# Kernel optimization log

Measured on AMD Instinct MI355X. Metric: run time of the kernel, lower is better.

The kernel has to match this reference:

```python
import jax, jax.numpy as jnp
import numpy as np

B, S, D = 32, 1024, 128
NUM_VT = 32
MIN_DR, MAX_DR = 0.0, 30.0
MIN_SOG, MAX_SOG = 0.0, 40.0
MIN_ROT, MAX_ROT = -127.0, 127.0


def setup_inputs() -> dict:
    key = jax.random.key(0)
    ks = jax.random.split(key, 32)
    u = lambda k, lo, hi: jax.random.uniform(k, (B, S, 1), minval=lo, maxval=hi, dtype=jnp.float32)
    lon = u(ks[0], -180.0, 180.0)
    lat = u(ks[1], -90.0, 90.0)
    rot = u(ks[2], MIN_ROT, MAX_ROT)
    sog = u(ks[3], MIN_SOG, MAX_SOG)
    cog = u(ks[4], 0.0, 360.0)
    head = u(ks[5], 0.0, 360.0)
    vtype = jax.random.randint(ks[6], (B, S, 1), 0, NUM_VT).astype(jnp.float32)
    dr = u(ks[7], MIN_DR, MAX_DR)
    ais_data = jnp.concatenate([lon, lat, rot, sog, cog, head, vtype, dr], axis=-1)
    p = lambda k, shape: (jax.random.normal(k, shape, dtype=jnp.float32) * 0.05)
    return {
        "ais_data": ais_data,
        "W_lon1": p(ks[8], (2, D)), "b_lon1": p(ks[9], (D,)),
        "W_lon2": p(ks[10], (D, D)), "b_lon2": p(ks[11], (D,)),
        "W_lat1": p(ks[12], (2, D)), "b_lat1": p(ks[13], (D,)),
        "W_lat2": p(ks[14], (D, D)), "b_lat2": p(ks[15], (D,)),
        "W_cog": p(ks[16], (2, D)), "b_cog": p(ks[17], (D,)),
        "W_head": p(ks[18], (2, D)), "b_head": p(ks[19], (D,)),
        "W_dr": p(ks[20], (1, D)), "b_dr": p(ks[21], (D,)),
        "W_sog": p(ks[22], (1, D)), "b_sog": p(ks[23], (D,)),
        "W_rot": p(ks[24], (1, D)), "b_rot": p(ks[25], (D,)),
        "emb": p(ks[26], (NUM_VT, D)),
    }


def reference(ais_data, W_lon1, b_lon1, W_lon2, b_lon2, W_lat1, b_lat1, W_lat2, b_lat2,
              W_cog, b_cog, W_head, b_head, W_dr, b_dr, W_sog, b_sog, W_rot, b_rot, emb):
    deg2rad = jnp.pi / 180.0
    lon = ais_data[..., 0:1]
    lat = ais_data[..., 1:2]
    rot = ais_data[..., 2:3]
    sog = ais_data[..., 3:4]
    cog = ais_data[..., 4:5]
    head = ais_data[..., 5:6]
    vtype = ais_data[..., 6]
    dr = ais_data[..., 7:8]

    def coord(x, mask_val, W1, b1, W2, b2):
        # x: [b,s,1] degrees -> 2-layer MLP on [sin, cos]
        xr = x * deg2rad
        f = jnp.concatenate([jnp.sin(xr), jnp.cos(xr)], axis=-1)  # [b,s,2]
        e = jax.nn.relu(f @ W1 + b1) @ W2 + b2                    # [b,s,D]
        return jnp.where(x == mask_val, 0.0, e)

    def cyclical(x, W, b):
        xr = x * deg2rad - jnp.pi
        f = jnp.concatenate([jnp.sin(xr), jnp.cos(xr)], axis=-1)
        e = f @ W + b
        return jnp.where(x == -1.0, 0.0, e)

    def continuous(x, mn, mx, W, b):
        xn = 2.0 * (x - mn) / jnp.maximum(mx - mn, 1e-6) - 1.0
        e = jnp.tanh(xn @ W + b)
        return jnp.where(x == -1.0, 0.0, e)

    enc_lon = coord(lon, 181.0, W_lon1, b_lon1, W_lon2, b_lon2)
    enc_lat = coord(lat, 91.0, W_lat1, b_lat1, W_lat2, b_lat2)
    enc_rot = continuous(rot, MIN_ROT, MAX_ROT, W_rot, b_rot)
    enc_sog = continuous(sog, MIN_SOG, MAX_SOG, W_sog, b_sog)
    enc_cog = cyclical(cog, W_cog, b_cog)
    enc_head = cyclical(head, W_head, b_head)
    vt_idx = jax.lax.stop_gradient(vtype).astype(jnp.int32)
    enc_vt = emb[vt_idx]                                          # [b,s,D]
    enc_dr = continuous(dr, MIN_DR, MAX_DR, W_dr, b_dr)

    # order matches torch.cat((spatial(lon,lat), rot, sog, cog, heading, vessel_type, draught))
    out = jnp.stack([enc_lon, enc_lat, enc_rot, enc_sog, enc_cog, enc_head, enc_vt, enc_dr], axis=2)
    b, s = ais_data.shape[:2]
    return out.reshape(b, s, -1)  # [b, s, 8*D]
```

## Files before the change

kernel.cpp:

```cpp
#include <hip/hip_runtime.h>
#include <cstdint>

typedef short bf16x8 __attribute__((ext_vector_type(8)));
typedef float f32x4 __attribute__((ext_vector_type(4)));

#define D2R 0.017453292519943295f
#define PI_F 3.14159265838979323846f
#undef PI_F
#define PI_F 3.14159265358979323846f

__device__ __forceinline__ unsigned bf16r(float x) {
    unsigned u = __float_as_uint(x);
    return (u + 0x7fffu + ((u >> 16) & 1u)) >> 16;
}

__device__ __forceinline__ float tanh_fast(float x) {
    float e = __expf(2.0f * x);
    return 1.0f - 2.0f / (e + 1.0f);
}

__global__ __launch_bounds__(512, 4) void hae_kernel(
    const float* __restrict__ ais,
    const float* __restrict__ Wlon1, const float* __restrict__ blon1,
    const float* __restrict__ Wlon2, const float* __restrict__ blon2,
    const float* __restrict__ Wlat1, const float* __restrict__ blat1,
    const float* __restrict__ Wlat2, const float* __restrict__ blat2,
    const float* __restrict__ Wcog,  const float* __restrict__ bcog,
    const float* __restrict__ Whead, const float* __restrict__ bhead,
    const float* __restrict__ Wdr,   const float* __restrict__ bdr,
    const float* __restrict__ Wsog,  const float* __restrict__ bsog,
    const float* __restrict__ Wrot,  const float* __restrict__ brot,
    const float* __restrict__ emb,
    float* __restrict__ out)
{
    __shared__ unsigned short hlds[2][64][128];
    __shared__ float s_sin[2][64], s_cos[2][64], s_mask[2][64];
    __shared__ float s_xn[3][64], s_mxn[3][64];
    __shared__ float s_scyc[2][64], s_ccyc[2][64], s_mcyc[2][64];
    __shared__ int   s_vt[64];

    const int t = threadIdx.x;
    const int tok0 = blockIdx.x * 64;

    if (t < 64) {
        const float* a = ais + (size_t)(tok0 + t) * 8;
        f32x4 a0 = *(const f32x4*)a;
        f32x4 a1 = *(const f32x4*)(a + 4);
        float lon = a0[0], lat = a0[1], rot = a0[2], sog = a0[3];
        float cog = a1[0], head = a1[1], vt = a1[2], dr = a1[3];

        float lr = lon * D2R;
        s_sin[0][t] = __sinf(lr); s_cos[0][t] = __cosf(lr);
        s_mask[0][t] = (lon == 181.0f) ? 0.f : 1.f;
        float tr = lat * D2R;
        s_sin[1][t] = __sinf(tr); s_cos[1][t] = __cosf(tr);
        s_mask[1][t] = (lat == 91.0f) ? 0.f : 1.f;

        s_xn[0][t] = (rot + 127.0f) * (2.0f / 254.0f) - 1.0f;
        s_mxn[0][t] = (rot == -1.0f) ? 0.f : 1.f;
        s_xn[1][t] = sog * (2.0f / 40.0f) - 1.0f;
        s_mxn[1][t] = (sog == -1.0f) ? 0.f : 1.f;
        s_xn[2][t] = dr * (2.0f / 30.0f) - 1.0f;
        s_mxn[2][t] = (dr == -1.0f) ? 0.f : 1.f;

        float cr = cog * D2R - PI_F;
        s_scyc[0][t] = __sinf(cr); s_ccyc[0][t] = __cosf(cr);
        s_mcyc[0][t] = (cog == -1.0f) ? 0.f : 1.f;
        float hr = head * D2R - PI_F;
        s_scyc[1][t] = __sinf(hr); s_ccyc[1][t] = __cosf(hr);
        s_mcyc[1][t] = (head == -1.0f) ? 0.f : 1.f;
        s_vt[t] = (int)vt;
    }
    __syncthreads();

    {
        const int j0 = (t & 63) * 2;
        const int quad = t >> 6;
        float w00a = Wlon1[j0],       w00b = Wlon1[j0 + 1];
        float w01a = Wlon1[128 + j0], w01b = Wlon1[128 + j0 + 1];
        float b0a  = blon1[j0],       b0b  = blon1[j0 + 1];
        float w10a = Wlat1[j0],       w10b = Wlat1[j0 + 1];
        float w11a = Wlat1[128 + j0], w11b = Wlat1[128 + j0 + 1];
        float b1a  = blat1[j0],       b1b  = blat1[j0 + 1];
        char* base0 = (char*)&hlds[0][0][0];
        char* base1 = (char*)&hlds[1][0][0];
        #pragma unroll
        for (int p = 0; p < 8; ++p) {
            int i = quad + p * 8;
            int sw = (j0 * 2) ^ ((i & 7) << 4);
            float s0 = s_sin[0][i], c0 = s_cos[0][i];
            float h0 = fmaxf(fmaf(s0, w00a, fmaf(c0, w01a, b0a)), 0.f);
            float h1 = fmaxf(fmaf(s0, w00b, fmaf(c0, w01b, b0b)), 0.f);
            *(unsigned*)(base0 + i * 256 + sw) = bf16r(h0) | (bf16r(h1) << 16);
            float s1 = s_sin[1][i], c1 = s_cos[1][i];
            float g0 = fmaxf(fmaf(s1, w10a, fmaf(c1, w11a, b1a)), 0.f);
            float g1 = fmaxf(fmaf(s1, w10b, fmaf(c1, w11b, b1b)), 0.f);
            *(unsigned*)(base1 + i * 256 + sw) = bf16r(g0) | (bf16r(g1) << 16);
        }
    }

    {
        const int d4 = (t & 31) * 4;
        const int io = t >> 5;
        f32x4 wr  = *(const f32x4*)(Wrot + d4),        br_ = *(const f32x4*)(brot + d4);
        f32x4 wsg = *(const f32x4*)(Wsog + d4),        bs_ = *(const f32x4*)(bsog + d4);
        f32x4 wdd = *(const f32x4*)(Wdr + d4),         bd_ = *(const f32x4*)(bdr + d4);
        f32x4 wc0 = *(const f32x4*)(Wcog + d4),  wc1 = *(const f32x4*)(Wcog + 128 + d4),  bc_ = *(const f32x4*)(bcog + d4);
        f32x4 wh0 = *(const f32x4*)(Whead + d4), wh1 = *(const f32x4*)(Whead + 128 + d4), bh_ = *(const f32x4*)(bhead + d4);
        #pragma unroll
        for (int p = 0; p < 4; ++p) {
            int i = io + p * 16;
            float* ob = out + (size_t)(tok0 + i) * 1024;
            {
                float xn = s_xn[0][i], mk = s_mxn[0][i];
                f32x4 v;
                #pragma unroll
                for (int e = 0; e < 4; ++e) v[e] = tanh_fast(fmaf(xn, wr[e], br_[e])) * mk;
                *(f32x4*)(ob + 2 * 128 + d4) = v;
            }
            {
                float xn = s_xn[1][i], mk = s_mxn[1][i];
                f32x4 v;
                #pragma unroll
                for (int e = 0; e < 4; ++e) v[e] = tanh_fast(fmaf(xn, wsg[e], bs_[e])) * mk;
                *(f32x4*)(ob + 3 * 128 + d4) = v;
            }
            {
                float sc = s_scyc[0][i], cc = s_ccyc[0][i], mk = s_mcyc[0][i];
                f32x4 v;
                #pragma unroll
                for (int e = 0; e < 4; ++e) v[e] = fmaf(sc, wc0[e], fmaf(cc, wc1[e], bc_[e])) * mk;
                *(f32x4*)(ob + 4 * 128 + d4) = v;
            }
            {
                float sc = s_scyc[1][i], cc = s_ccyc[1][i], mk = s_mcyc[1][i];
                f32x4 v;
                #pragma unroll
                for (int e = 0; e < 4; ++e) v[e] = fmaf(sc, wh0[e], fmaf(cc, wh1[e], bh_[e])) * mk;
                *(f32x4*)(ob + 5 * 128 + d4) = v;
            }
            {
                f32x4 ev = *(const f32x4*)(emb + (size_t)s_vt[i] * 128 + d4);
                *(f32x4*)(ob + 6 * 128 + d4) = ev;
            }
            {
                float xn = s_xn[2][i], mk = s_mxn[2][i];
                f32x4 v;
                #pragma unroll
                for (int e = 0; e < 4; ++e) v[e] = tanh_fast(fmaf(xn, wdd[e], bd_[e])) * mk;
                *(f32x4*)(ob + 7 * 128 + d4) = v;
            }
        }
    }

    const int w  = t >> 6;
    const int l  = t & 63;
    const int c  = w & 1;
    const int nh = (w >> 1) & 1;
    const int dq = w >> 2;
    const float* W2  = c ? Wlat2 : Wlon2;
    const float* b2p = c ? blat2 : blon2;
    const int col = l & 15;
    const int q   = l >> 4;
    const int dbase0 = nh * 64 + dq * 32;

    bf16x8 afrag[2][4];
    f32x4  bb4[2];
    #pragma unroll
    for (int dt = 0; dt < 2; ++dt) {
        const int dbase = dbase0 + dt * 16;
        bb4[dt] = *(const f32x4*)(b2p + dbase + q * 4);
        #pragma unroll
        for (int ks = 0; ks < 4; ++ks) {
            bf16x8 af;
            #pragma unroll
            for (int e = 0; e < 8; ++e)
                af[e] = (short)bf16r(W2[(size_t)(ks * 32 + q * 8 + e) * 128 + dbase + col]);
            afrag[dt][ks] = af;
        }
    }
    __syncthreads();

    char* hb = (char*)&hlds[c][0][0];
    #pragma unroll
    for (int tt = 0; tt < 4; ++tt) {
        const int brow = tt * 16 + col;
        const int swr = (brow & 7) << 4;
        bf16x8 bfrag[4];
        #pragma unroll
        for (int ks = 0; ks < 4; ++ks) {
            int jb = (ks * 32 + q * 8) * 2;
            bfrag[ks] = *(bf16x8*)(hb + brow * 256 + (jb ^ swr));
        }
        const float msk = s_mask[c][brow];
        float* op = out + (size_t)(tok0 + brow) * 1024 + c * 128 + dbase0 + q * 4;
        #pragma unroll
        for (int dt = 0; dt < 2; ++dt) {
            f32x4 acc = (f32x4){0.f, 0.f, 0.f, 0.f};
            acc = __builtin_amdgcn_mfma_f32_16x16x32_bf16(afrag[dt][0], bfrag[0], acc, 0, 0, 0);
            acc = __builtin_amdgcn_mfma_f32_16x16x32_bf16(afrag[dt][1], bfrag[1], acc, 0, 0, 0);
            acc = __builtin_amdgcn_mfma_f32_16x16x32_bf16(afrag[dt][2], bfrag[2], acc, 0, 0, 0);
            acc = __builtin_amdgcn_mfma_f32_16x16x32_bf16(afrag[dt][3], bfrag[3], acc, 0, 0, 0);
            f32x4 v;
            #pragma unroll
            for (int r = 0; r < 4; ++r) v[r] = (acc[r] + bb4[dt][r]) * msk;
            *(f32x4*)(op + dt * 16) = v;
        }
    }
}

extern "C" void kernel_launch(void* const* d_in, const int* in_sizes, int n_in,
                              void* d_out, int out_size, void* d_ws, size_t ws_size,
                              hipStream_t stream) {
    (void)in_sizes; (void)n_in; (void)d_ws; (void)ws_size; (void)out_size;
    const float* ais   = (const float*)d_in[0];
    const float* Wlon1 = (const float*)d_in[1];
    const float* blon1 = (const float*)d_in[2];
    const float* Wlon2 = (const float*)d_in[3];
    const float* blon2 = (const float*)d_in[4];
    const float* Wlat1 = (const float*)d_in[5];
    const float* blat1 = (const float*)d_in[6];
    const float* Wlat2 = (const float*)d_in[7];
    const float* blat2 = (const float*)d_in[8];
    const float* Wcog  = (const float*)d_in[9];
    const float* bcog  = (const float*)d_in[10];
    const float* Whead = (const float*)d_in[11];
    const float* bhead = (const float*)d_in[12];
    const float* Wdr   = (const float*)d_in[13];
    const float* bdr   = (const float*)d_in[14];
    const float* Wsog  = (const float*)d_in[15];
    const float* bsog  = (const float*)d_in[16];
    const float* Wrot  = (const float*)d_in[17];
    const float* brot  = (const float*)d_in[18];
    const float* emb   = (const float*)d_in[19];
    float* out = (float*)d_out;

    hae_kernel<<<512, 512, 0, stream>>>(ais,
        Wlon1, blon1, Wlon2, blon2,
        Wlat1, blat1, Wlat2, blat2,
        Wcog, bcog, Whead, bhead,
        Wdr, bdr, Wsog, bsog, Wrot, brot,
        emb, out);
}
```

Measured before the change: 28.63 us.

## Stage MLP outputs through LDS to write full contiguous token rows

MFMA results for the lon/lat MLP are first held in registers, then written to a swizzled 64KB LDS buffer, and finally read back so that each thread group writes all eight feature segments of a token row contiguously. This replaces scattered 16-byte fragment stores with row-ordered coalesced stores. It adds two block barriers, larger LDS usage that may reduce occupancy, and more live registers.

```diff
diff --git a/kernel.cpp b/kernel.cpp
--- a/kernel.cpp
+++ b/kernel.cpp
@@ -5,8 +5,6 @@
 typedef float f32x4 __attribute__((ext_vector_type(4)));
 
 #define D2R 0.017453292519943295f
-#define PI_F 3.14159265838979323846f
-#undef PI_F
 #define PI_F 3.14159265358979323846f
 
 __device__ __forceinline__ unsigned bf16r(float x) {
@@ -33,7 +31,7 @@
     const float* __restrict__ emb,
     float* __restrict__ out)
 {
-    __shared__ unsigned short hlds[2][64][128];
+    __shared__ __align__(16) char smem[65536];
     __shared__ float s_sin[2][64], s_cos[2][64], s_mask[2][64];
     __shared__ float s_xn[3][64], s_mxn[3][64];
     __shared__ float s_scyc[2][64], s_ccyc[2][64], s_mcyc[2][64];
@@ -82,8 +80,8 @@
         float w10a = Wlat1[j0],       w10b = Wlat1[j0 + 1];
         float w11a = Wlat1[128 + j0], w11b = Wlat1[128 + j0 + 1];
         float b1a  = blat1[j0],       b1b  = blat1[j0 + 1];
-        char* base0 = (char*)&hlds[0][0][0];
-        char* base1 = (char*)&hlds[1][0][0];
+        char* base0 = smem;
+        char* base1 = smem + 16384;
         #pragma unroll
         for (int p = 0; p < 8; ++p) {
             int i = quad + p * 8;
@@ -99,60 +97,6 @@
         }
     }
 
-    {
-        const int d4 = (t & 31) * 4;
-        const int io = t >> 5;
-        f32x4 wr  = *(const f32x4*)(Wrot + d4),        br_ = *(const f32x4*)(brot + d4);
-        f32x4 wsg = *(const f32x4*)(Wsog + d4),        bs_ = *(const f32x4*)(bsog + d4);
-        f32x4 wdd = *(const f32x4*)(Wdr + d4),         bd_ = *(const f32x4*)(bdr + d4);
-        f32x4 wc0 = *(const f32x4*)(Wcog + d4),  wc1 = *(const f32x4*)(Wcog + 128 + d4),  bc_ = *(const f32x4*)(bcog + d4);
-        f32x4 wh0 = *(const f32x4*)(Whead + d4), wh1 = *(const f32x4*)(Whead + 128 + d4), bh_ = *(const f32x4*)(bhead + d4);
-        #pragma unroll
-        for (int p = 0; p < 4; ++p) {
-            int i = io + p * 16;
-            float* ob = out + (size_t)(tok0 + i) * 1024;
-            {
-                float xn = s_xn[0][i], mk = s_mxn[0][i];
-                f32x4 v;
-                #pragma unroll
-                for (int e = 0; e < 4; ++e) v[e] = tanh_fast(fmaf(xn, wr[e], br_[e])) * mk;
-                *(f32x4*)(ob + 2 * 128 + d4) = v;
-            }
-            {
-                float xn = s_xn[1][i], mk = s_mxn[1][i];
-                f32x4 v;
-                #pragma unroll
-                for (int e = 0; e < 4; ++e) v[e] = tanh_fast(fmaf(xn, wsg[e], bs_[e])) * mk;
-                *(f32x4*)(ob + 3 * 128 + d4) = v;
-            }
-            {
-                float sc = s_scyc[0][i], cc = s_ccyc[0][i], mk = s_mcyc[0][i];
-                f32x4 v;
-                #pragma unroll
-                for (int e = 0; e < 4; ++e) v[e] = fmaf(sc, wc0[e], fmaf(cc, wc1[e], bc_[e])) * mk;
-                *(f32x4*)(ob + 4 * 128 + d4) = v;
-            }
-            {
-                float sc = s_scyc[1][i], cc = s_ccyc[1][i], mk = s_mcyc[1][i];
-                f32x4 v;
-                #pragma unroll
-                for (int e = 0; e < 4; ++e) v[e] = fmaf(sc, wh0[e], fmaf(cc, wh1[e], bh_[e])) * mk;
-                *(f32x4*)(ob + 5 * 128 + d4) = v;
-            }
-            {
-                f32x4 ev = *(const f32x4*)(emb + (size_t)s_vt[i] * 128 + d4);
-                *(f32x4*)(ob + 6 * 128 + d4) = ev;
-            }
-            {
-                float xn = s_xn[2][i], mk = s_mxn[2][i];
-                f32x4 v;
-                #pragma unroll
-                for (int e = 0; e < 4; ++e) v[e] = tanh_fast(fmaf(xn, wdd[e], bd_[e])) * mk;
-                *(f32x4*)(ob + 7 * 128 + d4) = v;
-            }
-        }
-    }
-
     const int w  = t >> 6;
     const int l  = t & 63;
     const int c  = w & 1;
@@ -181,30 +125,108 @@
     }
     __syncthreads();
 
-    char* hb = (char*)&hlds[c][0][0];
+    f32x4 vout[4][2];
+    {
+        char* hb = smem + c * 16384;
+        #pragma unroll
+        for (int tt = 0; tt < 4; ++tt) {
+            const int brow = tt * 16 + col;
+            const int swr = (brow & 7) << 4;
+            bf16x8 bfrag[4];
+            #pragma unroll
+            for (int ks = 0; ks < 4; ++ks) {
+                int jb = (ks * 32 + q * 8) * 2;
+                bfrag[ks] = *(bf16x8*)(hb + brow * 256 + (jb ^ swr));
+            }
+            const float msk = s_mask[c][brow];
+            #pragma unroll
+            for (int dt = 0; dt < 2; ++dt) {
+                f32x4 acc = (f32x4){0.f, 0.f, 0.f, 0.f};
+                acc = __builtin_amdgcn_mfma_f32_16x16x32_bf16(afrag[dt][0], bfrag[0], acc, 0, 0, 0);
+                acc = __builtin_amdgcn_mfma_f32_16x16x32_bf16(afrag[dt][1], bfrag[1], acc, 0, 0, 0);
+                acc = __builtin_amdgcn_mfma_f32_16x16x32_bf16(afrag[dt][2], bfrag[2], acc, 0, 0, 0);
+                acc = __builtin_amdgcn_mfma_f32_16x16x32_bf16(afrag[dt][3], bfrag[3], acc, 0, 0, 0);
+                f32x4 v;
+                #pragma unroll
+                for (int r = 0; r < 4; ++r) v[r] = (acc[r] + bb4[dt][r]) * msk;
+                vout[tt][dt] = v;
+            }
+        }
+    }
+    __syncthreads();
+
     #pragma unroll
     for (int tt = 0; tt < 4; ++tt) {
         const int brow = tt * 16 + col;
-        const int swr = (brow & 7) << 4;
-        bf16x8 bfrag[4];
-        #pragma unroll
-        for (int ks = 0; ks < 4; ++ks) {
-            int jb = (ks * 32 + q * 8) * 2;
-            bfrag[ks] = *(bf16x8*)(hb + brow * 256 + (jb ^ swr));
-        }
-        const float msk = s_mask[c][brow];
-        float* op = out + (size_t)(tok0 + brow) * 1024 + c * 128 + dbase0 + q * 4;
         #pragma unroll
         for (int dt = 0; dt < 2; ++dt) {
-            f32x4 acc = (f32x4){0.f, 0.f, 0.f, 0.f};
-            acc = __builtin_amdgcn_mfma_f32_16x16x32_bf16(afrag[dt][0], bfrag[0], acc, 0, 0, 0);
-            acc = __builtin_amdgcn_mfma_f32_16x16x32_bf16(afrag[dt][1], bfrag[1], acc, 0, 0, 0);
-            acc = __builtin_amdgcn_mfma_f32_16x16x32_bf16(afrag[dt][2], bfrag[2], acc, 0, 0, 0);
-            acc = __builtin_amdgcn_mfma_f32_16x16x32_bf16(afrag[dt][3], bfrag[3], acc, 0, 0, 0);
-            f32x4 v;
-            #pragma unroll
-            for (int r = 0; r < 4; ++r) v[r] = (acc[r] + bb4[dt][r]) * msk;
-            *(f32x4*)(op + dt * 16) = v;
+            int dbyte = (dbase0 + dt * 16 + q * 4) * 4;
+            *(f32x4*)(smem + c * 32768 + brow * 512 + (dbyte ^ ((brow & 7) << 4))) = vout[tt][dt];
+        }
+    }
+    __syncthreads();
+
+    {
+        const int j  = t & 31;
+        const int hw = t >> 5;
+        const int d4 = j * 4;
+        f32x4 wr  = *(const f32x4*)(Wrot + d4),        br_ = *(const f32x4*)(brot + d4);
+        f32x4 wsg = *(const f32x4*)(Wsog + d4),        bs_ = *(const f32x4*)(bsog + d4);
+        f32x4 wdd = *(const f32x4*)(Wdr + d4),         bd_ = *(const f32x4*)(bdr + d4);
+        f32x4 wc0 = *(const f32x4*)(Wcog + d4),  wc1 = *(const f32x4*)(Wcog + 128 + d4),  bc_ = *(const f32x4*)(bcog + d4);
+        f32x4 wh0 = *(const f32x4*)(Whead + d4), wh1 = *(const f32x4*)(Whead + 128 + d4), bh_ = *(const f32x4*)(bhead + d4);
+        #pragma unroll
+        for (int n = 0; n < 4; ++n) {
+            const int i = hw * 4 + n;
+            float* ob = out + (size_t)(tok0 + i) * 1024;
+            const int esw = (d4 * 4) ^ ((i & 7) << 4);
+            {
+                f32x4 v = *(const f32x4*)(smem + i * 512 + esw);
+                *(f32x4*)(ob + 0 * 128 + d4) = v;
+            }
+            {
+                f32x4 v = *(const f32x4*)(smem + 32768 + i * 512 + esw);
+                *(f32x4*)(ob + 1 * 128 + d4) = v;
+            }
+            {
+                float xn = s_xn[0][i], mk = s_mxn[0][i];
+                f32x4 v;
+                #pragma unroll
+                for (int e = 0; e < 4; ++e) v[e] = tanh_fast(fmaf(xn, wr[e], br_[e])) * mk;
+                *(f32x4*)(ob + 2 * 128 + d4) = v;
+            }
+            {
+                float xn = s_xn[1][i], mk = s_mxn[1][i];
+                f32x4 v;
+                #pragma unroll
+                for (int e = 0; e < 4; ++e) v[e] = tanh_fast(fmaf(xn, wsg[e], bs_[e])) * mk;
+                *(f32x4*)(ob + 3 * 128 + d4) = v;
+            }
+            {
+                float sc = s_scyc[0][i], cc = s_ccyc[0][i], mk = s_mcyc[0][i];
+                f32x4 v;
+                #pragma unroll
+                for (int e = 0; e < 4; ++e) v[e] = fmaf(sc, wc0[e], fmaf(cc, wc1[e], bc_[e])) * mk;
+                *(f32x4*)(ob + 4 * 128 + d4) = v;
+            }
+            {
+                float sc = s_scyc[1][i], cc = s_ccyc[1][i], mk = s_mcyc[1][i];
+                f32x4 v;
+                #pragma unroll
+                for (int e = 0; e < 4; ++e) v[e] = fmaf(sc, wh0[e], fmaf(cc, wh1[e], bh_[e])) * mk;
+                *(f32x4*)(ob + 5 * 128 + d4) = v;
+            }
+            {
+                f32x4 ev = *(const f32x4*)(emb + (size_t)s_vt[i] * 128 + d4);
+                *(f32x4*)(ob + 6 * 128 + d4) = ev;
+            }
+            {
+                float xn = s_xn[2][i], mk = s_mxn[2][i];
+                f32x4 v;
+                #pragma unroll
+                for (int e = 0; e < 4; ++e) v[e] = tanh_fast(fmaf(xn, wdd[e], bd_[e])) * mk;
+                *(f32x4*)(ob + 7 * 128 + d4) = v;
+            }
         }
     }
 }
```

Measured after the change: 32.02 us. 11.9% more time.
